# Kernel optimization log

Measured on AMD Instinct MI355X. Metric: run time of the kernel, lower is better.

The kernel has to match this reference:

```python
import jax, jax.numpy as jnp
import numpy as np

WS, OWS, NH = 16, 24, 2          # window size, overlap window size (=int(16*0.5)+16), num heads
PAD = (OWS - WS) // 2            # unfold padding = 4


def conv2d(x, w, b):
    kh, kw = w.shape[2], w.shape[3]
    out = jax.lax.conv_general_dilated(x, w, (1, 1), [(kh // 2, kh // 2), (kw // 2, kw // 2)],
                                       dimension_numbers=('NCHW', 'OIHW', 'NCHW'))
    return out + b[None, :, None, None]


def layer_norm(x, g, b, eps=1e-5):
    m = x.mean(-1, keepdims=True)
    v = ((x - m) ** 2).mean(-1, keepdims=True)
    return (x - m) * jax.lax.rsqrt(v + eps) * g + b


def stem(depth, cw1, cb1, cw2, cb2, cw3, cb3, cw4, cb4, in_g, in_b):
    # BasicConv(1->8,k3,relu) -> (8->16,k1,relu) -> (16->16,k3,relu) -> (16->32,k1) -> InstanceNorm2d(32,affine)
    y = jax.nn.relu(conv2d(depth, cw1, cb1))
    y = jax.nn.relu(conv2d(y, cw2, cb2))
    y = jax.nn.relu(conv2d(y, cw3, cb3))
    y = conv2d(y, cw4, cb4)
    m = y.mean((2, 3), keepdims=True)
    v = ((y - m) ** 2).mean((2, 3), keepdims=True)
    return (y - m) * jax.lax.rsqrt(v + 1e-5) * in_g[None, :, None, None] + in_b[None, :, None, None]


def ocab(xq, ykv, rpi, n1g, n1b, wq, bq, wkv, bkv, rpb, wp, bp, n2g, n2b, mw1, mb1, mw2, mb2):
    # Overlapping cross-attention block (HAT-style OCAB, cross variant: q from xq, kv from ykv).
    b, c, h, w = xq.shape
    x = xq.transpose(0, 2, 3, 1)   # b h w c
    y = ykv.transpose(0, 2, 3, 1)
    shortcut = x
    q = layer_norm(x, n1g, n1b) @ wq + bq          # b h w c
    kv = layer_norm(y, n1g, n1b) @ wkv + bkv       # b h w 2c
    nhw, nww = h // WS, w // WS
    # non-overlapping query windows: (b*nw, WS*WS, c)
    qw = q.reshape(b, nhw, WS, nww, WS, c).transpose(0, 1, 3, 2, 4, 5).reshape(b * nhw * nww, WS * WS, c)
    # overlapping kv windows via unfold (patch channel order = (channel, kh, kw), same as torch unfold)
    patches = jax.lax.conv_general_dilated_patches(kv.transpose(0, 3, 1, 2), (OWS, OWS), (WS, WS),
                                                   [(PAD, PAD), (PAD, PAD)])  # b, 2c*OWS*OWS, nhw, nww
    patches = patches.reshape(b, 2, c, OWS * OWS, nhw * nww).transpose(1, 0, 4, 3, 2).reshape(2, b * nhw * nww, OWS * OWS, c)
    k, v = patches[0], patches[1]
    d = c // NH
    qh = qw.reshape(-1, WS * WS, NH, d).transpose(0, 2, 1, 3) * (d ** -0.5)
    kh = k.reshape(-1, OWS * OWS, NH, d).transpose(0, 2, 1, 3)
    vh = v.reshape(-1, OWS * OWS, NH, d).transpose(0, 2, 1, 3)
    attn = jnp.einsum('whqd,whkd->whqk', qh, kh)
    attn = attn + rpb[rpi].transpose(2, 0, 1)[None]  # rel-pos bias -> [1, NH, WS*WS, OWS*OWS]
    attn = jax.nn.softmax(attn, axis=-1)
    out = jnp.einsum('whqk,whkd->whqd', attn, vh).transpose(0, 2, 1, 3).reshape(-1, WS * WS, c)
    # window reverse
    out = out.reshape(b, nhw, nww, WS, WS, c).transpose(0, 1, 3, 2, 4, 5).reshape(b, h, w, c)
    out = out @ wp + bp + shortcut
    out = out + (jax.nn.gelu(layer_norm(out, n2g, n2b) @ mw1 + mb1) @ mw2 + mb2)  # mlp_ratio=2
    return out.transpose(0, 3, 1, 2)


def setup_inputs():
    key = jax.random.key(0)
    ks = jax.random.split(key, 16)
    B, C, H, W = 1, 32, 256, 256
    s = 0.05
    return dict(
        x=jax.random.normal(ks[0], (B, C, H, W), jnp.float32),
        depth=jax.random.normal(ks[1], (B, 1, H, W), jnp.float32),
        rpi=jax.random.randint(ks[2], (WS * WS, OWS * OWS), 0, (WS + OWS - 1) ** 2),
        cw1=jax.random.normal(ks[3], (8, 1, 3, 3)) * s, cb1=jnp.zeros(8),
        cw2=jax.random.normal(ks[4], (16, 8, 1, 1)) * s, cb2=jnp.zeros(16),
        cw3=jax.random.normal(ks[5], (16, 16, 3, 3)) * s, cb3=jnp.zeros(16),
        cw4=jax.random.normal(ks[6], (32, 16, 1, 1)) * s, cb4=jnp.zeros(32),
        in_g=jnp.ones(32), in_b=jnp.zeros(32),
        n1g=jnp.ones(C), n1b=jnp.zeros(C),
        wq=jax.random.normal(ks[7], (C, C)) * s, bq=jnp.zeros(C),
        wkv=jax.random.normal(ks[8], (C, 2 * C)) * s, bkv=jnp.zeros(2 * C),
        rpb=jax.random.normal(ks[9], ((WS + OWS - 1) ** 2, NH)) * 0.02,
        wp=jax.random.normal(ks[10], (C, C)) * s, bp=jnp.zeros(C),
        n2g=jnp.ones(C), n2b=jnp.zeros(C),
        mw1=jax.random.normal(ks[11], (C, 2 * C)) * s, mb1=jnp.zeros(2 * C),
        mw2=jax.random.normal(ks[12], (2 * C, C)) * s, mb2=jnp.zeros(C),
    )


def reference(x, depth, rpi, cw1, cb1, cw2, cb2, cw3, cb3, cw4, cb4, in_g, in_b,
              n1g, n1b, wq, bq, wkv, bkv, rpb, wp, bp, n2g, n2b, mw1, mb1, mw2, mb2):
    f = stem(depth, cw1, cb1, cw2, cb2, cw3, cb3, cw4, cb4, in_g, in_b)
    a = (n1g, n1b, wq, bq, wkv, bkv, rpb, wp, bp, n2g, n2b, mw1, mb1, mw2, mb2)
    out1 = ocab(x, f, rpi, *a)   # shared OCAB weights, called twice with swapped roles
    out2 = ocab(f, x, rpi, *a)
    return out1 + out2 + x
```

## Files before the change

### kernel.cpp

```cpp
#include <hip/hip_runtime.h>
#include <hip/hip_bf16.h>

#define HW 65536
#define KPAD 584

typedef __attribute__((ext_vector_type(8))) short bf8;
typedef __attribute__((ext_vector_type(4))) float f4;

__device__ __forceinline__ unsigned short f2b(float x) {
  unsigned int u = __float_as_uint(x);
  unsigned int r = (u + 0x7fff + ((u >> 16) & 1)) >> 16;
  return (unsigned short)r;
}
__device__ __forceinline__ unsigned int pk2(float lo, float hi) {
  return (__float_as_uint(hi) & 0xffff0000u) | (__float_as_uint(lo) >> 16);
}
__device__ __forceinline__ float ex2(float x) { return __builtin_amdgcn_exp2f(x); }

__device__ __forceinline__ void stem_front_body(
    int bx, int t, const float* __restrict__ depth,
    const float* __restrict__ cw1, const float* __restrict__ cb1,
    const float* __restrict__ cw2, const float* __restrict__ cb2,
    float* __restrict__ t2) {
  int p = bx * 256 + t;
  int y = p >> 8, x = p & 255;
  float in9[9];
#pragma unroll
  for (int ky = 0; ky < 3; ky++)
#pragma unroll
    for (int kx = 0; kx < 3; kx++) {
      int yy = y + ky - 1, xx = x + kx - 1;
      bool ok = ((unsigned)yy < 256u) && ((unsigned)xx < 256u);
      in9[ky*3+kx] = ok ? depth[yy*256+xx] : 0.f;
    }
  float t1[8];
#pragma unroll
  for (int o = 0; o < 8; o++) {
    float s = cb1[o];
#pragma unroll
    for (int i = 0; i < 9; i++) s += in9[i] * cw1[o*9+i];
    t1[o] = fmaxf(s, 0.f);
  }
#pragma unroll
  for (int o = 0; o < 16; o++) {
    float s = cb2[o];
#pragma unroll
    for (int ci = 0; ci < 8; ci++) s += t1[ci] * cw2[o*8+ci];
    t2[o*HW + p] = fmaxf(s, 0.f);
  }
}

__device__ __forceinline__ void bias_body(
    int bx, int t, const int* __restrict__ rpi,
    const float* __restrict__ rpb, float* __restrict__ biasT) {
  int idx = bx*256 + t;
  int hd = idx / 147456;
  int rem = idx - hd*147456;
  int qt = rem / 9216;
  int r2 = rem - qt*9216;
  int kb = r2 >> 6;
  int q16 = (r2 >> 2) & 15;
  int r = r2 & 3;
  int key = kb*4 + r;
  int qq = qt*16 + q16;
  biasT[idx] = (rpb[rpi[qq*576 + key]*2 + hd] - 8.0f) * 1.44269504f;
}

__device__ __forceinline__ void lnmm16_body(
    int role, int bx, int t,
    float* ws, float* gs, float* bs, float* b2s, float* as, float* bbs,
    const float* __restrict__ x, const float* __restrict__ t4,
    const float* __restrict__ part,
    const float* __restrict__ ig, const float* __restrict__ ib,
    const float* __restrict__ n1g, const float* __restrict__ n1b,
    const float* __restrict__ wq, const float* __restrict__ bq,
    const float* __restrict__ wkv, const float* __restrict__ bkv,
    float* q1, float* kv1, float* q2, float* kv2) {
  const float *src, *wm, *bo; float* dst;
  int wstride, wcol; bool ain;
  if (role < 6) { src = x;  ain = false; } else { src = t4; ain = true; }
  switch (role) {
    default:
    case 0:  wm=wq;  wstride=32; wcol=0;  bo=bq;  dst=q1;               break;
    case 1:  wm=wq;  wstride=32; wcol=16; bo=bq;  dst=q1+16*HW;         break;
    case 2: case 3: case 4: case 5:
             wm=wkv; wstride=64; wcol=16*(role-2); bo=bkv; dst=kv2+16*(role-2)*HW; break;
    case 6:  wm=wq;  wstride=32; wcol=0;  bo=bq;  dst=q2;               break;
    case 7:  wm=wq;  wstride=32; wcol=16; bo=bq;  dst=q2+16*HW;         break;
    case 8: case 9: case 10: case 11:
             wm=wkv; wstride=64; wcol=16*(role-8); bo=bkv; dst=kv1+16*(role-8)*HW; break;
  }
  for (int i = t; i < 512; i += 256) ws[i] = wm[(i>>4)*wstride + wcol + (i&15)];
  if (t < 16) b2s[t] = bo[wcol + t];
  if (t < 32) {
    gs[t] = n1g[t]; bs[t] = n1b[t];
    if (ain) {
      float s = 0.f, ss = 0.f;
#pragma unroll
      for (int k = 0; k < 16; k++) { s += part[t*16+k]; ss += part[512 + t*16+k]; }
      float m = s * (1.f/65536.f);
      float var = ss * (1.f/65536.f) - m*m;
      float a = rsqrtf(var + 1e-5f) * ig[t];
      as[t] = a; bbs[t] = ib[t] - m*a;
    }
  }
  __syncthreads();
  int p = bx*256 + t;
  float v[32]; float s = 0.f;
  if (ain) {
#pragma unroll
    for (int c = 0; c < 32; c++) { v[c] = src[c*HW+p]*as[c] + bbs[c]; s += v[c]; }
  } else {
#pragma unroll
    for (int c = 0; c < 32; c++) { v[c] = src[c*HW+p]; s += v[c]; }
  }
  float m = s * 0.03125f;
  float ss = 0.f;
#pragma unroll
  for (int c = 0; c < 32; c++) { float d = v[c]-m; ss += d*d; }
  float rs = rsqrtf(ss*0.03125f + 1e-5f);
  float acc[16];
#pragma unroll
  for (int j = 0; j < 16; j++) acc[j] = b2s[j];
#pragma unroll
  for (int c = 0; c < 32; c++) {
    float ln = (v[c]-m)*rs*gs[c] + bs[c];
    const float4* w4 = (const float4*)&ws[c*16];
#pragma unroll
    for (int j4 = 0; j4 < 4; j4++) {
      float4 w = w4[j4];
      acc[j4*4+0] += ln*w.x; acc[j4*4+1] += ln*w.y;
      acc[j4*4+2] += ln*w.z; acc[j4*4+3] += ln*w.w;
    }
  }
#pragma unroll
  for (int j = 0; j < 16; j++) dst[j*HW+p] = acc[j];
}

__global__ __launch_bounds__(256) void k_misc(
    const float* __restrict__ depth,
    const float* __restrict__ cw1, const float* __restrict__ cb1,
    const float* __restrict__ cw2, const float* __restrict__ cb2,
    float* __restrict__ t2,
    const int* __restrict__ rpi, const float* __restrict__ rpb, float* __restrict__ biasT,
    const float* __restrict__ x, const float* __restrict__ t4, const float* __restrict__ part,
    const float* __restrict__ ig, const float* __restrict__ ib,
    const float* __restrict__ n1g, const float* __restrict__ n1b,
    const float* __restrict__ wq, const float* __restrict__ bq,
    const float* __restrict__ wkv, const float* __restrict__ bkv,
    float* q1, float* kv1, float* q2, float* kv2) {
  __shared__ __align__(16) float ws[512];
  __shared__ float gs[32], bs[32], b2s[16], as[32], bbs[32];
  int id = blockIdx.x, t = threadIdx.x;
  if (id < 256) { stem_front_body(id, t, depth, cw1, cb1, cw2, cb2, t2); return; }
  if (id < 1408) { bias_body(id - 256, t, rpi, rpb, biasT); return; }
  int r = id - 1408;
  lnmm16_body(r >> 8, r & 255, t, ws, gs, bs, b2s, as, bbs,
              x, t4, part, ig, ib, n1g, n1b, wq, bq, wkv, bkv, q1, kv1, q2, kv2);
}

__global__ __launch_bounds__(256) void k_lnmmB(
    const float* __restrict__ x, const float* __restrict__ t4, const float* __restrict__ part,
    const float* __restrict__ ig, const float* __restrict__ ib,
    const float* __restrict__ n1g, const float* __restrict__ n1b,
    const float* __restrict__ wq, const float* __restrict__ bq,
    const float* __restrict__ wkv, const float* __restrict__ bkv,
    float* q1, float* kv1, float* q2, float* kv2, int ybase) {
  __shared__ __align__(16) float ws[512];
  __shared__ float gs[32], bs[32], b2s[16], as[32], bbs[32];
  lnmm16_body(ybase + blockIdx.y, blockIdx.x, threadIdx.x, ws, gs, bs, b2s, as, bbs,
              x, t4, part, ig, ib, n1g, n1b, wq, bq, wkv, bkv, q1, kv1, q2, kv2);
}

__global__ __launch_bounds__(256) void k_conv3(
    const float* __restrict__ t2, const float* __restrict__ cw3,
    const float* __restrict__ cb3, float* __restrict__ t3) {
  int t = threadIdx.x;
  int p = blockIdx.x*256 + t;
  int og = blockIdx.y;
  int y = p >> 8, x = p & 255;
  float acc[4];
#pragma unroll
  for (int o = 0; o < 4; o++) acc[o] = cb3[og*4+o];
#pragma unroll 1
  for (int tap = 0; tap < 9; tap++) {
    int ky = tap/3 - 1, kx = tap - (tap/3)*3 - 1;
    int yy = y+ky, xx = x+kx;
    bool ok = ((unsigned)yy < 256u) && ((unsigned)xx < 256u);
    int pp = yy*256+xx;
#pragma unroll
    for (int ci = 0; ci < 16; ci++) {
      float v = ok ? t2[ci*HW+pp] : 0.f;
#pragma unroll
      for (int o = 0; o < 4; o++)
        acc[o] += v * cw3[(og*4+o)*144 + ci*9 + tap];
    }
  }
#pragma unroll
  for (int o = 0; o < 4; o++) t3[(og*4+o)*HW+p] = fmaxf(acc[o], 0.f);
}

__global__ __launch_bounds__(256) void k_conv4(
    const float* __restrict__ t3, const float* __restrict__ cw4,
    const float* __restrict__ cb4, float* __restrict__ t4) {
  int t = threadIdx.x;
  int p = blockIdx.x*256 + t;
  int og = blockIdx.y;
  float v[16];
#pragma unroll
  for (int ci = 0; ci < 16; ci++) v[ci] = t3[ci*HW+p];
#pragma unroll
  for (int o = 0; o < 8; o++) {
    int oo = og*8 + o;
    float s = cb4[oo];
#pragma unroll
    for (int ci = 0; ci < 16; ci++) s += v[ci]*cw4[oo*16+ci];
    t4[oo*HW+p] = s;
  }
}

__global__ __launch_bounds__(256) void k_instats1(const float* __restrict__ t4,
                                                  float* __restrict__ part) {
  int c = blockIdx.x >> 4, seg = blockIdx.x & 15;
  const float4* src = (const float4*)(t4 + c*HW + seg*4096);
  float s = 0.f, ss = 0.f;
  for (int i = threadIdx.x; i < 1024; i += 256) {
    float4 v = src[i];
    s  += v.x + v.y + v.z + v.w;
    ss += v.x*v.x + v.y*v.y + v.z*v.z + v.w*v.w;
  }
#pragma unroll
  for (int off = 32; off > 0; off >>= 1) {
    s  += __shfl_down(s, off, 64);
    ss += __shfl_down(ss, off, 64);
  }
  __shared__ float sh[8];
  int wid = threadIdx.x >> 6;
  if ((threadIdx.x & 63) == 0) { sh[wid] = s; sh[4+wid] = ss; }
  __syncthreads();
  if (threadIdx.x == 0) {
    part[blockIdx.x]       = sh[0]+sh[1]+sh[2]+sh[3];
    part[512 + blockIdx.x] = sh[4]+sh[5]+sh[6]+sh[7];
  }
}

__global__ __launch_bounds__(256, 4) void k_attn(
    const float* __restrict__ qA, const float* __restrict__ kvA, float* __restrict__ aoA,
    const float* __restrict__ qB, const float* __restrict__ kvB, float* __restrict__ aoB,
    const float* __restrict__ biasT) {
  __shared__ __align__(16) unsigned short Ks[576*16];
  __shared__ __align__(16) unsigned short Vt[16*KPAD];

  const float* q  = blockIdx.y ? qB  : qA;
  const float* kv = blockIdx.y ? kvB : kvA;
  float* ao       = blockIdx.y ? aoB : aoA;

  int id = blockIdx.x;
  int lin = ((id & 7) << 6) | (id >> 3);
  int wi = lin >> 1, hd = lin & 1;
  int wy = wi >> 4, wx = wi & 15;
  int t = threadIdx.x;
  int by = wy*16 - 4, bx = wx*16 - 4;
  int kbase = hd*16*HW, vbase = (32 + hd*16)*HW;

  int wave = t >> 6, lane = t & 63;
  int quad = lane >> 4, l16 = lane & 15;
  const bf8 zero8 = {0,0,0,0,0,0,0,0};

  bf8 qf[4];
#pragma unroll
  for (int qi = 0; qi < 4; qi++) {
    int qt = wave*4 + qi;
    if (quad < 2) {
      int prow = (wy*16 + qt)*256 + wx*16 + l16;
      unsigned short qtmp[8];
#pragma unroll
      for (int j = 0; j < 8; j++)
        qtmp[j] = f2b(q[(hd*16 + quad*8 + j)*HW + prow] * 0.360673503f);
      qf[qi] = *(const bf8*)qtmp;
    } else {
      qf[qi] = zero8;
    }
  }

  for (int e = t; e < 576; e += 256) {
    int dy = e / 24, dx = e - dy*24;
    int yy = by + dy, xx = bx + dx;
    bool ok = ((unsigned)yy < 256u) && ((unsigned)xx < 256u);
    int pp = yy*256 + xx;
    int off = e & 31;
    int ppos = ((off & 12) << 1) + ((off >> 4) << 2) + (off & 3);
    int vcol = (e & ~31) + ppos;
    unsigned short tk[16];
#pragma unroll
    for (int i = 0; i < 16; i++) {
      float kvl = ok ? kv[kbase + i*HW + pp] : 0.f;
      float vvl = ok ? kv[vbase + i*HW + pp] : 0.f;
      tk[i] = f2b(kvl);
      Vt[i*KPAD + vcol] = f2b(vvl);
    }
    *(uint4*)&Ks[e*16]     = *(uint4*)&tk[0];
    *(uint4*)&Ks[e*16 + 8] = *(uint4*)&tk[8];
  }
  __syncthreads();

  f4 oacc[4];
  float lr[4];
  const float* bb[4];
#pragma unroll
  for (int qi = 0; qi < 4; qi++) {
    int qt = wave*4 + qi;
    oacc[qi] = (f4){0.f,0.f,0.f,0.f};
    lr[qi] = 0.f;
    bb[qi] = biasT + (hd*16 + qt)*9216 + quad*64 + l16*4;
  }

#pragma unroll 2
  for (int kt2 = 0; kt2 < 18; kt2++) {
    int k0 = kt2 * 32;
    bf8 kf0 = zero8, kf1 = zero8;
    if (quad < 2) {
      kf0 = *(const bf8*)&Ks[(k0 + l16)*16 + quad*8];
      kf1 = *(const bf8*)&Ks[(k0 + 16 + l16)*16 + quad*8];
    }
    bf8 vf = *(const bf8*)&Vt[l16*KPAD + k0 + quad*8];
#pragma unroll
    for (int qi = 0; qi < 4; qi++) {
      f4 b0 = *(const f4*)&bb[qi][k0*16];
      f4 b1 = *(const f4*)&bb[qi][(k0+16)*16];
      f4 s0 = __builtin_amdgcn_mfma_f32_16x16x32_bf16(kf0, qf[qi], b0, 0, 0, 0);
      f4 s1 = __builtin_amdgcn_mfma_f32_16x16x32_bf16(kf1, qf[qi], b1, 0, 0, 0);
      float p0[4], p1[4];
#pragma unroll
      for (int r = 0; r < 4; r++) {
        p0[r] = ex2(s0[r]);
        p1[r] = ex2(s1[r]);
        lr[qi] += p0[r] + p1[r];
      }
      union { unsigned int u[4]; bf8 v; } P;
      P.u[0] = pk2(p0[0], p0[1]); P.u[1] = pk2(p0[2], p0[3]);
      P.u[2] = pk2(p1[0], p1[1]); P.u[3] = pk2(p1[2], p1[3]);
      oacc[qi] = __builtin_amdgcn_mfma_f32_16x16x32_bf16(P.v, vf, oacc[qi], 0, 0, 0);
    }
  }
#pragma unroll
  for (int qi = 0; qi < 4; qi++) {
    lr[qi] += __shfl_xor(lr[qi], 16, 64);
    lr[qi] += __shfl_xor(lr[qi], 32, 64);
  }
#pragma unroll
  for (int qi = 0; qi < 4; qi++) {
    int qt = wave*4 + qi;
#pragma unroll
    for (int r = 0; r < 4; r++) {
      float lv = __shfl(lr[qi], quad*4 + r, 64);
      int qw = qt*16 + quad*4 + r;
      ao[(hd*16 + l16)*HW + (wy*16 + (qw >> 4))*256 + wx*16 + (qw & 15)] = oacc[qi][r] / lv;
    }
  }
}

__global__ __launch_bounds__(256) void k_projmlp(
    const float* __restrict__ ao1, const float* __restrict__ ao2,
    const float* __restrict__ x, const float* __restrict__ t4,
    const float* __restrict__ part,
    const float* __restrict__ ig, const float* __restrict__ ib,
    const float* __restrict__ wp, const float* __restrict__ bp,
    const float* __restrict__ n2g, const float* __restrict__ n2b,
    const float* __restrict__ mw1, const float* __restrict__ mb1,
    const float* __restrict__ mw2, const float* __restrict__ mb2,
    float* __restrict__ o1, float* __restrict__ o2, int obase) {
  int oc = blockIdx.y + obase;
  const float* ao = oc ? ao2 : ao1;
  float* dst      = oc ? o2  : o1;
  __shared__ __align__(16) float wps[1024];
  __shared__ __align__(16) float w1s[2048];
  __shared__ __align__(16) float w2s[2048];
  __shared__ float bps[32], b1s[64], b2s[32], gs[32], bs[32], as[32], bbs[32];
  int t = threadIdx.x;
  for (int i = t; i < 1024; i += 256) wps[i] = wp[i];
  for (int i = t; i < 2048; i += 256) { w1s[i] = mw1[i]; w2s[i] = mw2[i]; }
  if (t < 64) b1s[t] = mb1[t];
  if (t < 32) {
    bps[t] = bp[t]; b2s[t] = mb2[t]; gs[t] = n2g[t]; bs[t] = n2b[t];
    float s = 0.f, ss = 0.f;
#pragma unroll
    for (int k = 0; k < 16; k++) { s += part[t*16+k]; ss += part[512 + t*16+k]; }
    float m = s * (1.f/65536.f);
    float var = ss * (1.f/65536.f) - m*m;
    float a = rsqrtf(var + 1e-5f) * ig[t];
    as[t] = a; bbs[t] = ib[t] - m*a;
  }
  __syncthreads();
  int p = blockIdx.x*256 + t;
  float acc[32];
#pragma unroll
  for (int j = 0; j < 32; j++) acc[j] = bps[j];
#pragma unroll
  for (int c = 0; c < 32; c++) {
    float vc = ao[c*HW+p];
    const float4* w4 = (const float4*)&wps[c*32];
#pragma unroll
    for (int j4 = 0; j4 < 8; j4++) {
      float4 w = w4[j4];
      acc[j4*4+0] += vc*w.x; acc[j4*4+1] += vc*w.y;
      acc[j4*4+2] += vc*w.z; acc[j4*4+3] += vc*w.w;
    }
  }
  if (oc == 0) {
#pragma unroll
    for (int j = 0; j < 32; j++) acc[j] += x[j*HW+p];
  } else {
#pragma unroll
    for (int j = 0; j < 32; j++) acc[j] += t4[j*HW+p]*as[j] + bbs[j];
  }
  float s = 0.f;
#pragma unroll
  for (int j = 0; j < 32; j++) s += acc[j];
  float m = s * 0.03125f;
  float ss = 0.f;
#pragma unroll
  for (int j = 0; j < 32; j++) { float d = acc[j]-m; ss += d*d; }
  float rs = rsqrtf(ss*0.03125f + 1e-5f);
  float r[32];
#pragma unroll
  for (int j = 0; j < 32; j++) r[j] = b2s[j];
#pragma unroll 1
  for (int half = 0; half < 2; half++) {
    float h[32];
#pragma unroll
    for (int k = 0; k < 32; k++) h[k] = b1s[half*32 + k];
#pragma unroll
    for (int c = 0; c < 32; c++) {
      float ln = (acc[c] - m) * rs * gs[c] + bs[c];
      const float4* w4 = (const float4*)&w1s[c*64 + half*32];
#pragma unroll
      for (int k4 = 0; k4 < 8; k4++) {
        float4 w = w4[k4];
        h[k4*4+0] += ln*w.x; h[k4*4+1] += ln*w.y; h[k4*4+2] += ln*w.z; h[k4*4+3] += ln*w.w;
      }
    }
#pragma unroll
    for (int k = 0; k < 32; k++) {
      float xx = h[k];
      float u = 0.7978845608f * (xx + 0.044715f*xx*xx*xx);
      float th = 1.f - 2.f/(1.f + __expf(2.f*u));
      h[k] = 0.5f * xx * (1.f + th);
    }
#pragma unroll
    for (int k = 0; k < 32; k++) {
      float hk = h[k];
      const float4* w4 = (const float4*)&w2s[(half*32 + k)*32];
#pragma unroll
      for (int j4 = 0; j4 < 8; j4++) {
        float4 w = w4[j4];
        r[j4*4+0] += hk*w.x; r[j4*4+1] += hk*w.y; r[j4*4+2] += hk*w.z; r[j4*4+3] += hk*w.w;
      }
    }
  }
#pragma unroll
  for (int j = 0; j < 32; j++) dst[j*HW + p] = acc[j] + r[j];
}

__global__ __launch_bounds__(256) void k_final(
    const float* o1, const float* __restrict__ o2,
    const float* __restrict__ x, float* out) {
  int i = blockIdx.x*256 + threadIdx.x;
  float4 a = ((const float4*)o1)[i];
  float4 b = ((const float4*)o2)[i];
  float4 c = ((const float4*)x)[i];
  float4 r;
  r.x = a.x + b.x + c.x; r.y = a.y + b.y + c.y;
  r.z = a.z + b.z + c.z; r.w = a.w + b.w + c.w;
  ((float4*)out)[i] = r;
}

extern "C" void kernel_launch(void* const* d_in, const int* in_sizes, int n_in,
                              void* d_out, int out_size, void* d_ws, size_t ws_size,
                              hipStream_t stream) {
  const float* x    = (const float*)d_in[0];
  const float* depth= (const float*)d_in[1];
  const int*   rpi  = (const int*)d_in[2];
  const float* cw1  = (const float*)d_in[3],  *cb1 = (const float*)d_in[4];
  const float* cw2  = (const float*)d_in[5],  *cb2 = (const float*)d_in[6];
  const float* cw3  = (const float*)d_in[7],  *cb3 = (const float*)d_in[8];
  const float* cw4  = (const float*)d_in[9],  *cb4 = (const float*)d_in[10];
  const float* in_g = (const float*)d_in[11], *in_b = (const float*)d_in[12];
  const float* n1g  = (const float*)d_in[13], *n1b = (const float*)d_in[14];
  const float* wq   = (const float*)d_in[15], *bq  = (const float*)d_in[16];
  const float* wkv  = (const float*)d_in[17], *bkv = (const float*)d_in[18];
  const float* rpb  = (const float*)d_in[19];
  const float* wp   = (const float*)d_in[20], *bp  = (const float*)d_in[21];
  const float* n2g  = (const float*)d_in[22], *n2b = (const float*)d_in[23];
  const float* mw1  = (const float*)d_in[24], *mb1 = (const float*)d_in[25];
  const float* mw2  = (const float*)d_in[26], *mb2 = (const float*)d_in[27];

  float* W   = (float*)d_ws;
  float* o1  = (float*)d_out;

  bool big = ws_size >= (size_t)85100000;

  if (big) {
    float* t4    = W;
    float* q1    = W + 2097152;
    float* q2    = W + 4194304;
    float* kv1   = W + 6291456;
    float* kv2   = W + 10485760;
    float* ao1   = W + 14680064;
    float* ao2   = W + 16777216;
    float* o2    = W + 18874368;
    float* biasT = W + 20971520;
    float* part  = W + 21266432;
    float* t2 = ao1, *t3 = q2;

    k_misc   <<<2944, 256, 0, stream>>>(depth, cw1, cb1, cw2, cb2, t2,
                                        rpi, rpb, biasT,
                                        x, t4, part, in_g, in_b, n1g, n1b,
                                        wq, bq, wkv, bkv, q1, kv1, q2, kv2);
    k_conv3  <<<dim3(256,4), 256, 0, stream>>>(t2, cw3, cb3, t3);
    k_conv4  <<<dim3(256,4), 256, 0, stream>>>(t3, cw4, cb4, t4);
    k_instats1<<<512, 256, 0, stream>>>(t4, part);
    k_lnmmB  <<<dim3(256,6), 256, 0, stream>>>(x, t4, part, in_g, in_b, n1g, n1b,
                                               wq, bq, wkv, bkv, q1, kv1, q2, kv2, 6);
    k_attn   <<<dim3(512,2), 256, 0, stream>>>(q1, kv1, ao1, q2, kv2, ao2, biasT);
    k_projmlp<<<dim3(256,2), 256, 0, stream>>>(ao1, ao2, x, t4, part, in_g, in_b,
                                               wp, bp, n2g, n2b, mw1, mb1, mw2, mb2,
                                               o1, o2, 0);
    k_final  <<<2048, 256, 0, stream>>>(o1, o2, x, o1);
  } else {
    float* t4    = W;
    float* q1    = W + 2097152;
    float* kv1   = W + 4194304;
    float* ao1   = W + 8388608;
    float* o2    = W + 10485760;
    float* biasT = W + 12582912;
    float* part  = W + 12877824;
    float* t2 = ao1, *t3 = o2;

    k_misc   <<<1920, 256, 0, stream>>>(depth, cw1, cb1, cw2, cb2, t2,
                                        rpi, rpb, biasT,
                                        x, t4, part, in_g, in_b, n1g, n1b,
                                        wq, bq, wkv, bkv, q1, kv1, q1, kv1);
    k_conv3  <<<dim3(256,4), 256, 0, stream>>>(t2, cw3, cb3, t3);
    k_conv4  <<<dim3(256,4), 256, 0, stream>>>(t3, cw4, cb4, t4);
    k_instats1<<<512, 256, 0, stream>>>(t4, part);
    k_lnmmB  <<<dim3(256,4), 256, 0, stream>>>(x, t4, part, in_g, in_b, n1g, n1b,
                                               wq, bq, wkv, bkv, q1, kv1, q1, kv1, 8);
    k_attn   <<<dim3(512,1), 256, 0, stream>>>(q1, kv1, ao1, q1, kv1, ao1, biasT);
    k_projmlp<<<dim3(256,1), 256, 0, stream>>>(ao1, ao1, x, t4, part, in_g, in_b,
                                               wp, bp, n2g, n2b, mw1, mb1, mw2, mb2,
                                               o1, o2, 0);
    k_lnmmB  <<<dim3(256,6), 256, 0, stream>>>(x, t4, part, in_g, in_b, n1g, n1b,
                                               wq, bq, wkv, bkv, q1, kv1, q1, kv1, 2);
    k_attn   <<<dim3(512,1), 256, 0, stream>>>(q1, kv1, ao1, q1, kv1, ao1, biasT);
    k_projmlp<<<dim3(256,1), 256, 0, stream>>>(ao1, ao1, x, t4, part, in_g, in_b,
                                               wp, bp, n2g, n2b, mw1, mb1, mw2, mb2,
                                               o1, o2, 1);
    k_final  <<<2048, 256, 0, stream>>>(o1, o2, x, o1);
  }
}
```

Measured before the change: 261.7 us.

## Store q/kv as packed bf16 from a widened 48-column LN-matmul

The LayerNorm+projection kernel now computes 48 output columns per block instead of 16, so each input pixel is normalised fewer times. It writes q (pre-scaled) and kv as packed round-to-nearest bf16 pairs. The attention kernel loads these packed words directly instead of converting fp32 to bf16 on the fly, which halves intermediate traffic and removes the small-workspace code path so both OCAB passes run in one batched launch. It also adds s_setprio around the MFMA loop. Trade-offs are higher register pressure from 48 accumulators and a changed intermediate memory layout.

```diff
diff --git a/kernel.cpp b/kernel.cpp
--- a/kernel.cpp
+++ b/kernel.cpp
@@ -14,6 +14,9 @@
 }
 __device__ __forceinline__ unsigned int pk2(float lo, float hi) {
   return (__float_as_uint(hi) & 0xffff0000u) | (__float_as_uint(lo) >> 16);
+}
+__device__ __forceinline__ unsigned int pkrne(float lo, float hi) {
+  return ((unsigned int)f2b(hi) << 16) | (unsigned int)f2b(lo);
 }
 __device__ __forceinline__ float ex2(float x) { return __builtin_amdgcn_exp2f(x); }
 
@@ -66,32 +69,29 @@
   biasT[idx] = (rpb[rpi[qq*576 + key]*2 + hd] - 8.0f) * 1.44269504f;
 }
 
-__device__ __forceinline__ void lnmm16_body(
+__device__ __forceinline__ void lnmm48_body(
     int role, int bx, int t,
-    float* ws, float* gs, float* bs, float* b2s, float* as, float* bbs,
+    float* ws, float* gs, float* bs, float* b2s, float* as_, float* bbs_,
     const float* __restrict__ x, const float* __restrict__ t4,
     const float* __restrict__ part,
     const float* __restrict__ ig, const float* __restrict__ ib,
     const float* __restrict__ n1g, const float* __restrict__ n1b,
     const float* __restrict__ wq, const float* __restrict__ bq,
     const float* __restrict__ wkv, const float* __restrict__ bkv,
-    float* q1, float* kv1, float* q2, float* kv2) {
-  const float *src, *wm, *bo; float* dst;
-  int wstride, wcol; bool ain;
-  if (role < 6) { src = x;  ain = false; } else { src = t4; ain = true; }
-  switch (role) {
-    default:
-    case 0:  wm=wq;  wstride=32; wcol=0;  bo=bq;  dst=q1;               break;
-    case 1:  wm=wq;  wstride=32; wcol=16; bo=bq;  dst=q1+16*HW;         break;
-    case 2: case 3: case 4: case 5:
-             wm=wkv; wstride=64; wcol=16*(role-2); bo=bkv; dst=kv2+16*(role-2)*HW; break;
-    case 6:  wm=wq;  wstride=32; wcol=0;  bo=bq;  dst=q2;               break;
-    case 7:  wm=wq;  wstride=32; wcol=16; bo=bq;  dst=q2+16*HW;         break;
-    case 8: case 9: case 10: case 11:
-             wm=wkv; wstride=64; wcol=16*(role-8); bo=bkv; dst=kv1+16*(role-8)*HW; break;
-  }
-  for (int i = t; i < 512; i += 256) ws[i] = wm[(i>>4)*wstride + wcol + (i&15)];
-  if (t < 16) b2s[t] = bo[wcol + t];
+    unsigned int* __restrict__ q1, unsigned int* __restrict__ kv1,
+    unsigned int* __restrict__ q2, unsigned int* __restrict__ kv2) {
+  const float QS = 0.360673503f;
+  bool ain = role >= 2;
+  int slice = role & 1;
+  const float* src = ain ? t4 : x;
+  unsigned int* dq  = ain ? q2 : q1;
+  unsigned int* dkv = ain ? kv1 : kv2;
+  for (int i = t; i < 1536; i += 256) {
+    int c = i / 48, j = i - c*48;
+    ws[i] = slice ? wkv[c*64 + 16 + j]
+                  : (j < 32 ? wq[c*32 + j] : wkv[c*64 + (j - 32)]);
+  }
+  if (t < 48) b2s[t] = slice ? bkv[16 + t] : (t < 32 ? bq[t] : bkv[t - 32]);
   if (t < 32) {
     gs[t] = n1g[t]; bs[t] = n1b[t];
     if (ain) {
@@ -101,7 +101,7 @@
       float m = s * (1.f/65536.f);
       float var = ss * (1.f/65536.f) - m*m;
       float a = rsqrtf(var + 1e-5f) * ig[t];
-      as[t] = a; bbs[t] = ib[t] - m*a;
+      as_[t] = a; bbs_[t] = ib[t] - m*a;
     }
   }
   __syncthreads();
@@ -109,7 +109,7 @@
   float v[32]; float s = 0.f;
   if (ain) {
 #pragma unroll
-    for (int c = 0; c < 32; c++) { v[c] = src[c*HW+p]*as[c] + bbs[c]; s += v[c]; }
+    for (int c = 0; c < 32; c++) { v[c] = src[c*HW+p]*as_[c] + bbs_[c]; s += v[c]; }
   } else {
 #pragma unroll
     for (int c = 0; c < 32; c++) { v[c] = src[c*HW+p]; s += v[c]; }
@@ -119,22 +119,32 @@
 #pragma unroll
   for (int c = 0; c < 32; c++) { float d = v[c]-m; ss += d*d; }
   float rs = rsqrtf(ss*0.03125f + 1e-5f);
-  float acc[16];
-#pragma unroll
-  for (int j = 0; j < 16; j++) acc[j] = b2s[j];
+  float acc[48];
+#pragma unroll
+  for (int j = 0; j < 48; j++) acc[j] = b2s[j];
 #pragma unroll
   for (int c = 0; c < 32; c++) {
     float ln = (v[c]-m)*rs*gs[c] + bs[c];
-    const float4* w4 = (const float4*)&ws[c*16];
-#pragma unroll
-    for (int j4 = 0; j4 < 4; j4++) {
+    const float4* w4 = (const float4*)&ws[c*48];
+#pragma unroll
+    for (int j4 = 0; j4 < 12; j4++) {
       float4 w = w4[j4];
       acc[j4*4+0] += ln*w.x; acc[j4*4+1] += ln*w.y;
       acc[j4*4+2] += ln*w.z; acc[j4*4+3] += ln*w.w;
     }
   }
-#pragma unroll
-  for (int j = 0; j < 16; j++) dst[j*HW+p] = acc[j];
+  if (slice == 0) {
+#pragma unroll
+    for (int j2 = 0; j2 < 16; j2++)
+      dq[j2*HW+p] = pkrne(acc[2*j2]*QS, acc[2*j2+1]*QS);
+#pragma unroll
+    for (int c2 = 0; c2 < 8; c2++)
+      dkv[c2*HW+p] = pkrne(acc[32+2*c2], acc[32+2*c2+1]);
+  } else {
+#pragma unroll
+    for (int c2 = 0; c2 < 24; c2++)
+      dkv[(8+c2)*HW+p] = pkrne(acc[2*c2], acc[2*c2+1]);
+  }
 }
 
 __global__ __launch_bounds__(256) void k_misc(
@@ -143,32 +153,34 @@
     const float* __restrict__ cw2, const float* __restrict__ cb2,
     float* __restrict__ t2,
     const int* __restrict__ rpi, const float* __restrict__ rpb, float* __restrict__ biasT,
-    const float* __restrict__ x, const float* __restrict__ t4, const float* __restrict__ part,
+    const float* __restrict__ x, const float* __restrict__ t4,
+    const float* __restrict__ part,
     const float* __restrict__ ig, const float* __restrict__ ib,
     const float* __restrict__ n1g, const float* __restrict__ n1b,
     const float* __restrict__ wq, const float* __restrict__ bq,
     const float* __restrict__ wkv, const float* __restrict__ bkv,
-    float* q1, float* kv1, float* q2, float* kv2) {
-  __shared__ __align__(16) float ws[512];
-  __shared__ float gs[32], bs[32], b2s[16], as[32], bbs[32];
+    unsigned int* q1, unsigned int* kv1, unsigned int* q2, unsigned int* kv2) {
+  __shared__ __align__(16) float ws[1536];
+  __shared__ float gs[32], bs[32], b2s[48], as_[32], bbs_[32];
   int id = blockIdx.x, t = threadIdx.x;
   if (id < 256) { stem_front_body(id, t, depth, cw1, cb1, cw2, cb2, t2); return; }
   if (id < 1408) { bias_body(id - 256, t, rpi, rpb, biasT); return; }
   int r = id - 1408;
-  lnmm16_body(r >> 8, r & 255, t, ws, gs, bs, b2s, as, bbs,
+  lnmm48_body(r >> 8, r & 255, t, ws, gs, bs, b2s, as_, bbs_,
               x, t4, part, ig, ib, n1g, n1b, wq, bq, wkv, bkv, q1, kv1, q2, kv2);
 }
 
 __global__ __launch_bounds__(256) void k_lnmmB(
-    const float* __restrict__ x, const float* __restrict__ t4, const float* __restrict__ part,
+    const float* __restrict__ x, const float* __restrict__ t4,
+    const float* __restrict__ part,
     const float* __restrict__ ig, const float* __restrict__ ib,
     const float* __restrict__ n1g, const float* __restrict__ n1b,
     const float* __restrict__ wq, const float* __restrict__ bq,
     const float* __restrict__ wkv, const float* __restrict__ bkv,
-    float* q1, float* kv1, float* q2, float* kv2, int ybase) {
-  __shared__ __align__(16) float ws[512];
-  __shared__ float gs[32], bs[32], b2s[16], as[32], bbs[32];
-  lnmm16_body(ybase + blockIdx.y, blockIdx.x, threadIdx.x, ws, gs, bs, b2s, as, bbs,
+    unsigned int* q1, unsigned int* kv1, unsigned int* q2, unsigned int* kv2) {
+  __shared__ __align__(16) float ws[1536];
+  __shared__ float gs[32], bs[32], b2s[48], as_[32], bbs_[32];
+  lnmm48_body(2 + blockIdx.y, blockIdx.x, threadIdx.x, ws, gs, bs, b2s, as_, bbs_,
               x, t4, part, ig, ib, n1g, n1b, wq, bq, wkv, bkv, q1, kv1, q2, kv2);
 }
 
@@ -245,15 +257,17 @@
 }
 
 __global__ __launch_bounds__(256, 4) void k_attn(
-    const float* __restrict__ qA, const float* __restrict__ kvA, float* __restrict__ aoA,
-    const float* __restrict__ qB, const float* __restrict__ kvB, float* __restrict__ aoB,
+    const unsigned int* __restrict__ qA, const unsigned int* __restrict__ kvA,
+    float* __restrict__ aoA,
+    const unsigned int* __restrict__ qB, const unsigned int* __restrict__ kvB,
+    float* __restrict__ aoB,
     const float* __restrict__ biasT) {
   __shared__ __align__(16) unsigned short Ks[576*16];
   __shared__ __align__(16) unsigned short Vt[16*KPAD];
 
-  const float* q  = blockIdx.y ? qB  : qA;
-  const float* kv = blockIdx.y ? kvB : kvA;
-  float* ao       = blockIdx.y ? aoB : aoA;
+  const unsigned int* q  = blockIdx.y ? qB  : qA;
+  const unsigned int* kv = blockIdx.y ? kvB : kvA;
+  float* ao              = blockIdx.y ? aoB : aoA;
 
   int id = blockIdx.x;
   int lin = ((id & 7) << 6) | (id >> 3);
@@ -261,7 +275,7 @@
   int wy = wi >> 4, wx = wi & 15;
   int t = threadIdx.x;
   int by = wy*16 - 4, bx = wx*16 - 4;
-  int kbase = hd*16*HW, vbase = (32 + hd*16)*HW;
+  int krow = hd*8, vrow = 16 + hd*8;
 
   int wave = t >> 6, lane = t & 63;
   int quad = lane >> 4, l16 = lane & 15;
@@ -270,14 +284,14 @@
   bf8 qf[4];
 #pragma unroll
   for (int qi = 0; qi < 4; qi++) {
-    int qt = wave*4 + qi;
     if (quad < 2) {
+      int qt = wave*4 + qi;
       int prow = (wy*16 + qt)*256 + wx*16 + l16;
-      unsigned short qtmp[8];
-#pragma unroll
-      for (int j = 0; j < 8; j++)
-        qtmp[j] = f2b(q[(hd*16 + quad*8 + j)*HW + prow] * 0.360673503f);
-      qf[qi] = *(const bf8*)qtmp;
+      union { unsigned int u[4]; bf8 v; } Q;
+#pragma unroll
+      for (int jw = 0; jw < 4; jw++)
+        Q.u[jw] = q[(krow + quad*4 + jw)*HW + prow];
+      qf[qi] = Q.v;
     } else {
       qf[qi] = zero8;
     }
@@ -291,16 +305,17 @@
     int off = e & 31;
     int ppos = ((off & 12) << 1) + ((off >> 4) << 2) + (off & 3);
     int vcol = (e & ~31) + ppos;
-    unsigned short tk[16];
-#pragma unroll
-    for (int i = 0; i < 16; i++) {
-      float kvl = ok ? kv[kbase + i*HW + pp] : 0.f;
-      float vvl = ok ? kv[vbase + i*HW + pp] : 0.f;
-      tk[i] = f2b(kvl);
-      Vt[i*KPAD + vcol] = f2b(vvl);
-    }
-    *(uint4*)&Ks[e*16]     = *(uint4*)&tk[0];
-    *(uint4*)&Ks[e*16 + 8] = *(uint4*)&tk[8];
+    unsigned int kwd[8];
+#pragma unroll
+    for (int i = 0; i < 8; i++) kwd[i] = ok ? kv[(krow + i)*HW + pp] : 0u;
+    *(uint4*)&Ks[e*16]     = *(const uint4*)&kwd[0];
+    *(uint4*)&Ks[e*16 + 8] = *(const uint4*)&kwd[4];
+#pragma unroll
+    for (int i = 0; i < 8; i++) {
+      unsigned int vw = ok ? kv[(vrow + i)*HW + pp] : 0u;
+      Vt[(2*i)*KPAD + vcol]   = (unsigned short)vw;
+      Vt[(2*i+1)*KPAD + vcol] = (unsigned short)(vw >> 16);
+    }
   }
   __syncthreads();
 
@@ -324,6 +339,7 @@
       kf1 = *(const bf8*)&Ks[(k0 + 16 + l16)*16 + quad*8];
     }
     bf8 vf = *(const bf8*)&Vt[l16*KPAD + k0 + quad*8];
+    __builtin_amdgcn_s_setprio(1);
 #pragma unroll
     for (int qi = 0; qi < 4; qi++) {
       f4 b0 = *(const f4*)&bb[qi][k0*16];
@@ -342,6 +358,7 @@
       P.u[2] = pk2(p1[0], p1[1]); P.u[3] = pk2(p1[2], p1[3]);
       oacc[qi] = __builtin_amdgcn_mfma_f32_16x16x32_bf16(P.v, vf, oacc[qi], 0, 0, 0);
     }
+    __builtin_amdgcn_s_setprio(0);
   }
 #pragma unroll
   for (int qi = 0; qi < 4; qi++) {
@@ -498,64 +515,31 @@
   float* W   = (float*)d_ws;
   float* o1  = (float*)d_out;
 
-  bool big = ws_size >= (size_t)85100000;
-
-  if (big) {
-    float* t4    = W;
-    float* q1    = W + 2097152;
-    float* q2    = W + 4194304;
-    float* kv1   = W + 6291456;
-    float* kv2   = W + 10485760;
-    float* ao1   = W + 14680064;
-    float* ao2   = W + 16777216;
-    float* o2    = W + 18874368;
-    float* biasT = W + 20971520;
-    float* part  = W + 21266432;
-    float* t2 = ao1, *t3 = q2;
-
-    k_misc   <<<2944, 256, 0, stream>>>(depth, cw1, cb1, cw2, cb2, t2,
-                                        rpi, rpb, biasT,
-                                        x, t4, part, in_g, in_b, n1g, n1b,
-                                        wq, bq, wkv, bkv, q1, kv1, q2, kv2);
-    k_conv3  <<<dim3(256,4), 256, 0, stream>>>(t2, cw3, cb3, t3);
-    k_conv4  <<<dim3(256,4), 256, 0, stream>>>(t3, cw4, cb4, t4);
-    k_instats1<<<512, 256, 0, stream>>>(t4, part);
-    k_lnmmB  <<<dim3(256,6), 256, 0, stream>>>(x, t4, part, in_g, in_b, n1g, n1b,
-                                               wq, bq, wkv, bkv, q1, kv1, q2, kv2, 6);
-    k_attn   <<<dim3(512,2), 256, 0, stream>>>(q1, kv1, ao1, q2, kv2, ao2, biasT);
-    k_projmlp<<<dim3(256,2), 256, 0, stream>>>(ao1, ao2, x, t4, part, in_g, in_b,
-                                               wp, bp, n2g, n2b, mw1, mb1, mw2, mb2,
-                                               o1, o2, 0);
-    k_final  <<<2048, 256, 0, stream>>>(o1, o2, x, o1);
-  } else {
-    float* t4    = W;
-    float* q1    = W + 2097152;
-    float* kv1   = W + 4194304;
-    float* ao1   = W + 8388608;
-    float* o2    = W + 10485760;
-    float* biasT = W + 12582912;
-    float* part  = W + 12877824;
-    float* t2 = ao1, *t3 = o2;
-
-    k_misc   <<<1920, 256, 0, stream>>>(depth, cw1, cb1, cw2, cb2, t2,
-                                        rpi, rpb, biasT,
-                                        x, t4, part, in_g, in_b, n1g, n1b,
-                                        wq, bq, wkv, bkv, q1, kv1, q1, kv1);
-    k_conv3  <<<dim3(256,4), 256, 0, stream>>>(t2, cw3, cb3, t3);
-    k_conv4  <<<dim3(256,4), 256, 0, stream>>>(t3, cw4, cb4, t4);
-    k_instats1<<<512, 256, 0, stream>>>(t4, part);
-    k_lnmmB  <<<dim3(256,4), 256, 0, stream>>>(x, t4, part, in_g, in_b, n1g, n1b,
-                                               wq, bq, wkv, bkv, q1, kv1, q1, kv1, 8);
-    k_attn   <<<dim3(512,1), 256, 0, stream>>>(q1, kv1, ao1, q1, kv1, ao1, biasT);
-    k_projmlp<<<dim3(256,1), 256, 0, stream>>>(ao1, ao1, x, t4, part, in_g, in_b,
-                                               wp, bp, n2g, n2b, mw1, mb1, mw2, mb2,
-                                               o1, o2, 0);
-    k_lnmmB  <<<dim3(256,6), 256, 0, stream>>>(x, t4, part, in_g, in_b, n1g, n1b,
-                                               wq, bq, wkv, bkv, q1, kv1, q1, kv1, 2);
-    k_attn   <<<dim3(512,1), 256, 0, stream>>>(q1, kv1, ao1, q1, kv1, ao1, biasT);
-    k_projmlp<<<dim3(256,1), 256, 0, stream>>>(ao1, ao1, x, t4, part, in_g, in_b,
-                                               wp, bp, n2g, n2b, mw1, mb1, mw2, mb2,
-                                               o1, o2, 1);
-    k_final  <<<2048, 256, 0, stream>>>(o1, o2, x, o1);
-  }
-}
+  float* t4    = W;
+  unsigned int* q1  = (unsigned int*)(W + 2097152);
+  unsigned int* q2  = (unsigned int*)(W + 3145728);
+  unsigned int* kv1 = (unsigned int*)(W + 4194304);
+  unsigned int* kv2 = (unsigned int*)(W + 6291456);
+  float* ao1   = W + 8388608;
+  float* ao2   = W + 10485760;
+  float* biasT = W + 12582912;
+  float* part  = W + 12877824;
+  float* t2 = ao1;
+  float* t3 = ao2;
+  float* o2 = W + 2097152;
+
+  k_misc   <<<1920, 256, 0, stream>>>(depth, cw1, cb1, cw2, cb2, t2,
+                                      rpi, rpb, biasT,
+                                      x, t4, part, in_g, in_b, n1g, n1b,
+                                      wq, bq, wkv, bkv, q1, kv1, q2, kv2);
+  k_conv3  <<<dim3(256,4), 256, 0, stream>>>(t2, cw3, cb3, t3);
+  k_conv4  <<<dim3(256,4), 256, 0, stream>>>(t3, cw4, cb4, t4);
+  k_instats1<<<512, 256, 0, stream>>>(t4, part);
+  k_lnmmB  <<<dim3(256,2), 256, 0, stream>>>(x, t4, part, in_g, in_b, n1g, n1b,
+                                             wq, bq, wkv, bkv, q1, kv1, q2, kv2);
+  k_attn   <<<dim3(512,2), 256, 0, stream>>>(q1, kv1, ao1, q2, kv2, ao2, biasT);
+  k_projmlp<<<dim3(256,2), 256, 0, stream>>>(ao1, ao2, x, t4, part, in_g, in_b,
+                                             wp, bp, n2g, n2b, mw1, mb1, mw2, mb2,
+                                             o1, o2, 0);
+  k_final  <<<2048, 256, 0, stream>>>(o1, o2, x, o1);
+}
```

Result: faster. 256.0 us (-2.2%).
